# Kernel optimization log

Hardware: AMD Instinct MI355X
Metric: run time of the kernel (lower is better)

The kernel has to match this reference:

```python
import jax, jax.numpy as jnp
import numpy as np

DIM = 256
K = 255
PAD = K // 2  # 127, 'same' padding


def _dwconv(x, w, b, pad_h, pad_w):
    # x: [N, C, H, W]; w: [C, 1, kh, kw] (OIHW with feature_group_count=C)
    y = jax.lax.conv_general_dilated(
        x, w,
        window_strides=(1, 1),
        padding=((pad_h, pad_h), (pad_w, pad_w)),
        dimension_numbers=("NCHW", "OIHW", "NCHW"),
        feature_group_count=x.shape[1],
    )
    return y + b[None, :, None, None]


def setup_inputs() -> dict:
    key = jax.random.key(0)
    k1, k2, k3, k4, k5 = jax.random.split(key, 5)
    x = jax.random.normal(k1, (10, DIM, 128, 128), dtype=jnp.float32)
    # depthwise weights, scaled like torch's kaiming-uniform fan_in=K
    scale = 1.0 / np.sqrt(K)
    wh = jax.random.uniform(k2, (DIM, 1, K, 1), jnp.float32, -scale, scale)
    bh = jax.random.uniform(k3, (DIM,), jnp.float32, -scale, scale)
    ww = jax.random.uniform(k4, (DIM, 1, 1, K), jnp.float32, -scale, scale)
    bw = jax.random.uniform(k5, (DIM,), jnp.float32, -scale, scale)
    return {"x": x, "wh": wh, "bh": bh, "ww": ww, "bw": bw}


def reference(x, wh, bh, ww, bw):
    # conv_h: (K,1) depthwise conv, padding (K//2, 0)
    x = _dwconv(x, wh, bh, PAD, 0)
    # conv_w: (1,K) depthwise conv, padding (0, K//2)
    x = _dwconv(x, ww, bw, 0, PAD)
    return x
```

## Files before the change

### kernel.cpp

```cpp
#include <hip/hip_runtime.h>

#define HW 128
#define KTAPS 255
#define DIMC 256

typedef short short8 __attribute__((ext_vector_type(8)));
typedef float f32x16 __attribute__((ext_vector_type(16)));

__device__ __forceinline__ short f2bf(float f) {
    return __builtin_bit_cast(short, (__bf16)f);
}
__device__ __forceinline__ int pad16(int c) { return c + (c >> 3); }


__global__ __launch_bounds__(256, 2)
void sep_conv255_mfma(const float* __restrict__ x,
                      const float* __restrict__ wh,
                      const float* __restrict__ bh,
                      const float* __restrict__ ww,
                      const float* __restrict__ bw,
                      float* __restrict__ out) {
    __shared__ __align__(16) short P1[2304 * 8];
    __shared__ __align__(16) short P2[2304 * 8];

    const int blk  = blockIdx.x;
    const int c    = blk & (DIMC - 1);
    const int tid  = threadIdx.x;
    const int lane = tid & 63;
    const int wv   = tid >> 6;

    const float* __restrict__ xc  = x + (size_t)blk * (HW * HW);
    float* __restrict__ zc        = out + (size_t)blk * (HW * HW);
    const float* __restrict__ whc = wh + c * KTAPS;
    const float* __restrict__ wwc = ww + c * KTAPS;

#pragma unroll
    for (int i = 0; i < 8; ++i) {
        const int ch = tid + (i << 8);
        const int lc = ch & 63;
        const int ks = (ch >> 6) & 7;
        const int tm = ch >> 9;
        const int m  = (tm << 5) + (lc & 31);
        const int kb = (ks << 4) + ((lc >> 5) << 3);
        const float* wp = whc + (127 + kb - m);
        short8 v;
#pragma unroll
        for (int j = 0; j < 8; ++j) v[j] = f2bf(wp[j]);
        *reinterpret_cast<short8*>(&P2[pad16(ch) * 8]) = v;
    }
    {
        const int n  = tid & 127;
        const int bc = (n >> 5) << 3;
#pragma unroll 2
        for (int i = 0; i < 8; ++i) {
            const int rg = (tid >> 7) + (i << 1);
            const int r0 = rg << 3;
            float xv[8];
#pragma unroll
            for (int j = 0; j < 8; ++j) xv[j] = xc[(r0 + j) * HW + n];
            short8 v;
#pragma unroll
            for (int j = 0; j < 8; ++j) v[j] = f2bf(xv[j]);
            const int ch = (bc + (r0 >> 4)) * 64 + (n & 31) + (((r0 >> 3) & 1) << 5);
            *reinterpret_cast<short8*>(&P1[pad16(ch) * 8]) = v;
        }
    }
    __syncthreads();

    f32x16 acc[4];
#pragma unroll
    for (int t = 0; t < 4; ++t)
#pragma unroll
        for (int j = 0; j < 16; ++j) acc[t][j] = 0.0f;

#pragma unroll
    for (int ks = 0; ks < 8; ++ks) {
        const short8 a = *reinterpret_cast<const short8*>(
            &P2[pad16(((wv << 3) + ks) * 64 + lane) * 8]);
#pragma unroll
        for (int t = 0; t < 4; ++t) {
            const short8 b = *reinterpret_cast<const short8*>(
                &P1[pad16(((t << 3) + ks) * 64 + lane) * 8]);
            acc[t] = __builtin_amdgcn_mfma_f32_32x32x16_bf16(a, b, acc[t], 0, 0, 0);
        }
    }
    __syncthreads();

    const float bhv = bh[c];
    {
        const int hbase = (wv << 5) + ((lane >> 5) << 2);
        const int s31   = lane & 31;
#pragma unroll
        for (int t = 0; t < 4; ++t) {
            const int s  = (t << 5) + s31;
            const int cb = ((wv << 3) + (s >> 4)) * 64 + (((s >> 3) & 1) << 5);
            const int jj = s & 7;
#pragma unroll
            for (int r = 0; r < 16; ++r) {
                const int h = hbase + (r & 3) + ((r >> 2) << 3);
                P1[pad16(cb + (h & 31)) * 8 + jj] = f2bf(acc[t][r] + bhv);
            }
        }
    }
#pragma unroll
    for (int i = 0; i < 8; ++i) {
        const int ch = tid + (i << 8);
        const int lc = ch & 63;
        const int ks = (ch >> 6) & 7;
        const int tn = ch >> 9;
        const int n  = (tn << 5) + (lc & 31);
        const int kb = (ks << 4) + ((lc >> 5) << 3);
        const float* wp = wwc + (127 + kb - n);
        short8 v;
#pragma unroll
        for (int j = 0; j < 8; ++j) v[j] = f2bf(wp[j]);
        *reinterpret_cast<short8*>(&P2[pad16(ch) * 8]) = v;
    }
    __syncthreads();

#pragma unroll
    for (int t = 0; t < 4; ++t)
#pragma unroll
        for (int j = 0; j < 16; ++j) acc[t][j] = 0.0f;

#pragma unroll
    for (int ks = 0; ks < 8; ++ks) {
        const short8 a = *reinterpret_cast<const short8*>(
            &P1[pad16(((wv << 3) + ks) * 64 + lane) * 8]);
#pragma unroll
        for (int t = 0; t < 4; ++t) {
            const short8 b = *reinterpret_cast<const short8*>(
                &P2[pad16(((t << 3) + ks) * 64 + lane) * 8]);
            acc[t] = __builtin_amdgcn_mfma_f32_32x32x16_bf16(a, b, acc[t], 0, 0, 0);
        }
    }

    const float bwv = bw[c];
    {
        const int hbase = (wv << 5) + ((lane >> 5) << 2);
        const int w31   = lane & 31;
#pragma unroll
        for (int t = 0; t < 4; ++t) {
            const int w2 = (t << 5) + w31;
#pragma unroll
            for (int r = 0; r < 16; ++r) {
                const int h = hbase + (r & 3) + ((r >> 2) << 3);
                zc[h * HW + w2] = acc[t][r] + bwv;
            }
        }
    }
}

extern "C" void kernel_launch(void* const* d_in, const int* in_sizes, int n_in,
                              void* d_out, int out_size, void* d_ws, size_t ws_size,
                              hipStream_t stream) {
    const float* x  = (const float*)d_in[0];
    const float* wh = (const float*)d_in[1];
    const float* bh = (const float*)d_in[2];
    const float* ww = (const float*)d_in[3];
    const float* bw = (const float*)d_in[4];
    float* outp = (float*)d_out;

    const int nbatch = in_sizes[0] / (DIMC * HW * HW);
    dim3 grid(nbatch * DIMC);
    dim3 block(256);
    hipLaunchKernelGGL(sep_conv255_mfma, grid, block, 0, stream,
                       x, wh, bh, ww, bw, outp);
}
```

Baseline: 295.3 us.

## Split per-channel work across 8 waves and prefetch width weights into registers

Doubles the block to 512 threads so each of 8 waves computes a 32x64 output tile (two MFMA accumulators) instead of 32x128, halving per-wave accumulator registers and MFMA serial chains. The width-conv weight band is now loaded and converted into registers before the first barrier, so its global-load latency overlaps the first GEMM instead of sitting between the two passes. This trades higher register pressure from the held weights and more waves contending for LDS against greater latency hiding.

```diff
diff --git a/kernel.cpp b/kernel.cpp
--- a/kernel.cpp
+++ b/kernel.cpp
@@ -13,7 +13,7 @@
 __device__ __forceinline__ int pad16(int c) { return c + (c >> 3); }
 
 
-__global__ __launch_bounds__(256, 2)
+__global__ __launch_bounds__(512, 4)
 void sep_conv255_mfma(const float* __restrict__ x,
                       const float* __restrict__ wh,
                       const float* __restrict__ bh,
@@ -28,6 +28,8 @@
     const int tid  = threadIdx.x;
     const int lane = tid & 63;
     const int wv   = tid >> 6;
+    const int wm   = wv >> 1;
+    const int wn   = wv & 1;
 
     const float* __restrict__ xc  = x + (size_t)blk * (HW * HW);
     float* __restrict__ zc        = out + (size_t)blk * (HW * HW);
@@ -35,8 +37,8 @@
     const float* __restrict__ wwc = ww + c * KTAPS;
 
 #pragma unroll
-    for (int i = 0; i < 8; ++i) {
-        const int ch = tid + (i << 8);
+    for (int i = 0; i < 4; ++i) {
+        const int ch = tid + (i << 9);
         const int lc = ch & 63;
         const int ks = (ch >> 6) & 7;
         const int tm = ch >> 9;
@@ -51,9 +53,9 @@
     {
         const int n  = tid & 127;
         const int bc = (n >> 5) << 3;
-#pragma unroll 2
-        for (int i = 0; i < 8; ++i) {
-            const int rg = (tid >> 7) + (i << 1);
+#pragma unroll
+        for (int i = 0; i < 4; ++i) {
+            const int rg = (tid >> 7) + (i << 2);
             const int r0 = rg << 3;
             float xv[8];
 #pragma unroll
@@ -65,87 +67,93 @@
             *reinterpret_cast<short8*>(&P1[pad16(ch) * 8]) = v;
         }
     }
+    short8 wreg[4];
+#pragma unroll
+    for (int i = 0; i < 4; ++i) {
+        const int ch = tid + (i << 9);
+        const int lc = ch & 63;
+        const int ks = (ch >> 6) & 7;
+        const int tn = ch >> 9;
+        const int nn = (tn << 5) + (lc & 31);
+        const int kb = (ks << 4) + ((lc >> 5) << 3);
+        const float* wp = wwc + (127 + kb - nn);
+#pragma unroll
+        for (int j = 0; j < 8; ++j) wreg[i][j] = f2bf(wp[j]);
+    }
     __syncthreads();
 
-    f32x16 acc[4];
+    f32x16 acc[2];
 #pragma unroll
-    for (int t = 0; t < 4; ++t)
+    for (int t = 0; t < 2; ++t)
 #pragma unroll
         for (int j = 0; j < 16; ++j) acc[t][j] = 0.0f;
 
 #pragma unroll
     for (int ks = 0; ks < 8; ++ks) {
         const short8 a = *reinterpret_cast<const short8*>(
-            &P2[pad16(((wv << 3) + ks) * 64 + lane) * 8]);
+            &P2[pad16(((wm << 3) + ks) * 64 + lane) * 8]);
 #pragma unroll
-        for (int t = 0; t < 4; ++t) {
+        for (int tt = 0; tt < 2; ++tt) {
+            const int t = (wn << 1) + tt;
             const short8 b = *reinterpret_cast<const short8*>(
                 &P1[pad16(((t << 3) + ks) * 64 + lane) * 8]);
-            acc[t] = __builtin_amdgcn_mfma_f32_32x32x16_bf16(a, b, acc[t], 0, 0, 0);
+            acc[tt] = __builtin_amdgcn_mfma_f32_32x32x16_bf16(a, b, acc[tt], 0, 0, 0);
         }
     }
     __syncthreads();
 
     const float bhv = bh[c];
+    const int hbase = (wm << 5) + ((lane >> 5) << 2);
     {
-        const int hbase = (wv << 5) + ((lane >> 5) << 2);
-        const int s31   = lane & 31;
+        const int s31 = lane & 31;
 #pragma unroll
-        for (int t = 0; t < 4; ++t) {
+        for (int tt = 0; tt < 2; ++tt) {
+            const int t  = (wn << 1) + tt;
             const int s  = (t << 5) + s31;
-            const int cb = ((wv << 3) + (s >> 4)) * 64 + (((s >> 3) & 1) << 5);
+            const int cb = ((wm << 3) + (s >> 4)) * 64 + (((s >> 3) & 1) << 5);
             const int jj = s & 7;
 #pragma unroll
             for (int r = 0; r < 16; ++r) {
                 const int h = hbase + (r & 3) + ((r >> 2) << 3);
-                P1[pad16(cb + (h & 31)) * 8 + jj] = f2bf(acc[t][r] + bhv);
+                P1[pad16(cb + (h & 31)) * 8 + jj] = f2bf(acc[tt][r] + bhv);
             }
         }
     }
 #pragma unroll
-    for (int i = 0; i < 8; ++i) {
-        const int ch = tid + (i << 8);
-        const int lc = ch & 63;
-        const int ks = (ch >> 6) & 7;
-        const int tn = ch >> 9;
-        const int n  = (tn << 5) + (lc & 31);
-        const int kb = (ks << 4) + ((lc >> 5) << 3);
-        const float* wp = wwc + (127 + kb - n);
-        short8 v;
-#pragma unroll
-        for (int j = 0; j < 8; ++j) v[j] = f2bf(wp[j]);
-        *reinterpret_cast<short8*>(&P2[pad16(ch) * 8]) = v;
+    for (int i = 0; i < 4; ++i) {
+        const int ch = tid + (i << 9);
+        *reinterpret_cast<short8*>(&P2[pad16(ch) * 8]) = wreg[i];
     }
     __syncthreads();
 
 #pragma unroll
-    for (int t = 0; t < 4; ++t)
+    for (int t = 0; t < 2; ++t)
 #pragma unroll
         for (int j = 0; j < 16; ++j) acc[t][j] = 0.0f;
 
 #pragma unroll
     for (int ks = 0; ks < 8; ++ks) {
         const short8 a = *reinterpret_cast<const short8*>(
-            &P1[pad16(((wv << 3) + ks) * 64 + lane) * 8]);
+            &P1[pad16(((wm << 3) + ks) * 64 + lane) * 8]);
 #pragma unroll
-        for (int t = 0; t < 4; ++t) {
+        for (int tt = 0; tt < 2; ++tt) {
+            const int t = (wn << 1) + tt;
             const short8 b = *reinterpret_cast<const short8*>(
                 &P2[pad16(((t << 3) + ks) * 64 + lane) * 8]);
-            acc[t] = __builtin_amdgcn_mfma_f32_32x32x16_bf16(a, b, acc[t], 0, 0, 0);
+            acc[tt] = __builtin_amdgcn_mfma_f32_32x32x16_bf16(a, b, acc[tt], 0, 0, 0);
         }
     }
 
     const float bwv = bw[c];
     {
-        const int hbase = (wv << 5) + ((lane >> 5) << 2);
-        const int w31   = lane & 31;
+        const int w31 = lane & 31;
 #pragma unroll
-        for (int t = 0; t < 4; ++t) {
-            const int w2 = (t << 5) + w31;
+        for (int tt = 0; tt < 2; ++tt) {
+            const int w2 = (((wn << 1) + tt) << 5) + w31;
 #pragma unroll
             for (int r = 0; r < 16; ++r) {
                 const int h = hbase + (r & 3) + ((r >> 2) << 3);
-                zc[h * HW + w2] = acc[t][r] + bwv;
+                zc[h * HW + w2] = acc[tt][r] + bwv;
             }
         }
     }
@@ -163,7 +171,7 @@
 
     const int nbatch = in_sizes[0] / (DIMC * HW * HW);
     dim3 grid(nbatch * DIMC);
-    dim3 block(256);
+    dim3 block(512);
     hipLaunchKernelGGL(sep_conv255_mfma, grid, block, 0, stream,
                        x, wh, bh, ww, bw, outp);
 }
```

Result: no change. 289.9 us (-1.8%).
